# Performance work log

Measured on AMD Instinct MI355X. Metric: run time of the kernel, lower is better.

The kernel has to match this reference:

```python
import jax, jax.numpy as jnp
import numpy as np

NV, NSEG, SEGSZ, GRID = 778, 16, 49, 32
SCALE_FACTOR = 0.1


def grid_sample_3d(vol, pts):
    """Trilinear grid_sample, align_corners=True, zeros padding.
    vol: [D,H,W]; pts: [N,3] with (x,y,z) in [-1,1] (x indexes W, z indexes D).
    """
    D, H, W = vol.shape
    fx = (pts[:, 0] + 1.0) * 0.5 * (W - 1)
    fy = (pts[:, 1] + 1.0) * 0.5 * (H - 1)
    fz = (pts[:, 2] + 1.0) * 0.5 * (D - 1)
    x0f, y0f, z0f = jnp.floor(fx), jnp.floor(fy), jnp.floor(fz)
    wx, wy, wz = fx - x0f, fy - y0f, fz - z0f
    x0 = x0f.astype(jnp.int32)
    y0 = y0f.astype(jnp.int32)
    z0 = z0f.astype(jnp.int32)
    out = jnp.zeros(pts.shape[0], vol.dtype)
    for dz in (0, 1):
        zz = z0 + dz
        ww_z = wz if dz else (1.0 - wz)
        for dy in (0, 1):
            yy = y0 + dy
            ww_zy = ww_z * (wy if dy else (1.0 - wy))
            for dx in (0, 1):
                xx = x0 + dx
                w = ww_zy * (wx if dx else (1.0 - wx))
                valid = (xx >= 0) & (xx < W) & (yy >= 0) & (yy < H) & (zz >= 0) & (zz < D)
                v = vol[jnp.clip(zz, 0, D - 1), jnp.clip(yy, 0, H - 1), jnp.clip(xx, 0, W - 1)]
                out = out + jnp.where(valid, v, 0.0) * w
    return out


def _boxes(segv):
    # segv: [B,16,S,3] -> center [B,16,3], scale [B,16]  (no_grad in original)
    mn = segv.min(axis=2)
    mx = segv.max(axis=2)
    center = 0.5 * (mn + mx)                       # mean of (min, max)
    scale = (1.0 + SCALE_FACTOR) * 0.5 * (mx - mn).max(axis=-1)
    return jax.lax.stop_gradient(center), jax.lax.stop_gradient(scale)


def _cross_sample(seg_src, center, scale, phi, seg):
    # seg_src [B,I,S,3]; center [B,J,3]; scale [B,J]; phi [J,B,G,G,G]
    B = seg_src.shape[0]
    coords = (seg_src[:, :, None, :, :] - center[:, None, :, None, :]) / scale[:, None, :, None, None]
    pts = coords.transpose(2, 0, 1, 3, 4).reshape(NSEG, B, NSEG * SEGSZ, 3)  # [J,B,M,3]
    vals = jax.vmap(jax.vmap(grid_sample_3d))(phi, pts)                      # [J,B,M]
    vals = vals.reshape(NSEG, B, NSEG, SEGSZ).transpose(1, 2, 0, 3)          # [B,I,J,S]
    phisum = vals.sum(axis=2)                                                # [B,I,S]
    orisum = (vals * scale[:, None, :, None]).sum(axis=2)                    # [B,I,S]
    flat = seg.reshape(-1)
    out = jnp.zeros((B, NV), jnp.float32).at[:, flat].add(phisum.reshape(B, -1))
    ori = jnp.zeros((B, NV), jnp.float32).at[:, flat].add(orisum.reshape(B, -1))
    return out, ori


def setup_inputs() -> dict:
    key = jax.random.key(0)
    k1, k2, k3, k4 = jax.random.split(key, 4)
    bs = 128
    vertices = jax.random.normal(k1, (bs, 2, NV, 3), dtype=jnp.float32)
    seg = jax.random.randint(k2, (NSEG, SEGSZ), 0, NV).astype(jnp.int32)
    phi_right = jax.random.uniform(k3, (NSEG, bs, GRID, GRID, GRID), dtype=jnp.float32)
    phi_left = jax.random.uniform(k4, (NSEG, bs, GRID, GRID, GRID), dtype=jnp.float32)
    return {"vertices": vertices, "phi_right": phi_right, "phi_left": phi_left, "seg": seg}


def reference(vertices, phi_right, phi_left, seg):
    left_vert = vertices[:, 1]   # [B,778,3]
    right_vert = vertices[:, 0]
    segL = left_vert[:, seg]     # [B,16,S,3]
    segR = right_vert[:, seg]
    cL, sL = _boxes(segL)
    cR, sR = _boxes(segR)
    out_left, _ = _cross_sample(segL, cR, sR, phi_right, seg)
    out_right, _ = _cross_sample(segR, cL, sL, phi_left, seg)
    num_hand = 2
    loss = (out_left / num_hand ** 2 + out_right / num_hand ** 2).sum(axis=1)  # [B]
    return loss
```

## Files before the change

### kernel.cpp

```cpp
#include <hip/hip_runtime.h>

#define NVV   778
#define NSEG  16
#define SEGSZ 49
#define GRIDN 32
#define BATCH 128
#define NPTS  (NSEG * SEGSZ)
#define VOLSZ (GRIDN * GRIDN * GRIDN)

__global__ __launch_bounds__(1024) void sample_kernel(
    const float* __restrict__ vertices, const int* __restrict__ seg,
    const float* __restrict__ phiR, const float* __restrict__ phiL,
    float* __restrict__ loss)
{
    __shared__ float vol[VOLSZ];
    __shared__ float wsum[16];
    __shared__ float sbox[4];

    int blk  = blockIdx.x;
    int k    = blk % NSEG;
    int b    = (blk / NSEG) % BATCH;
    int pass = blk / (NSEG * BATCH);
    int srcSide = (pass == 0) ? 1 : 0;
    int boxSide = 1 - srcSide;
    const float* phi = (pass == 0 ? phiR : phiL) +
                       ((size_t)k * BATCH + b) * VOLSZ;
    const float* vsrc = vertices + ((size_t)b * 2 + srcSide) * NVV * 3;
    const float* vbox = vertices + ((size_t)b * 2 + boxSide) * NVV * 3;

    const int tid = threadIdx.x;

    float4 stg[8];
    #pragma unroll
    for (int i = 0; i < 8; ++i)
        stg[i] = *(const float4*)(phi + ((i * 1024 + tid) << 2));

    if (tid < 64) {
        bool act = tid < SEGSZ;
        int vi = act ? seg[k * SEGSZ + tid] : 0;
        const float* v = vbox + (size_t)vi * 3;
        float x = v[0], y = v[1], z = v[2];
        float mnx = act ? x : 1e30f, mxx = act ? x : -1e30f;
        float mny = act ? y : 1e30f, mxy = act ? y : -1e30f;
        float mnz = act ? z : 1e30f, mxz = act ? z : -1e30f;
        #pragma unroll
        for (int m = 32; m; m >>= 1) {
            mnx = fminf(mnx, __shfl_xor(mnx, m));
            mxx = fmaxf(mxx, __shfl_xor(mxx, m));
            mny = fminf(mny, __shfl_xor(mny, m));
            mxy = fmaxf(mxy, __shfl_xor(mxy, m));
            mnz = fminf(mnz, __shfl_xor(mnz, m));
            mxz = fmaxf(mxz, __shfl_xor(mxz, m));
        }
        if (tid == 0) {
            sbox[0] = 0.5f * (mnx + mxx);
            sbox[1] = 0.5f * (mny + mxy);
            sbox[2] = 0.5f * (mnz + mxz);
            float ext = fmaxf(fmaxf(mxx - mnx, mxy - mny), mxz - mnz);
            sbox[3] = 1.0f / (0.55f * ext);
        }
    }

    float vx = 0.f, vy = 0.f, vz = 0.f;
    if (tid < NPTS) {
        int vi = seg[tid];
        const float* v = vsrc + (size_t)vi * 3;
        vx = v[0]; vy = v[1]; vz = v[2];
    }

    #pragma unroll
    for (int i = 0; i < 8; ++i)
        *(float4*)&vol[(i * 1024 + tid) << 2] = stg[i];

    __syncthreads();

    float acc = 0.0f;
    if (tid < NPTS) {
        float cx = sbox[0], cy = sbox[1], cz = sbox[2], invs = sbox[3];
        float fx = ((vx - cx) * invs + 1.0f) * 15.5f;
        float fy = ((vy - cy) * invs + 1.0f) * 15.5f;
        float fz = ((vz - cz) * invs + 1.0f) * 15.5f;
        if (!(fx <= -1.0f || fx >= 32.0f ||
              fy <= -1.0f || fy >= 32.0f ||
              fz <= -1.0f || fz >= 32.0f)) {
            float x0f = floorf(fx), y0f = floorf(fy), z0f = floorf(fz);
            float wx = fx - x0f, wy = fy - y0f, wz = fz - z0f;
            int x0 = (int)x0f, y0 = (int)y0f, z0 = (int)z0f;
            #pragma unroll
            for (int dz = 0; dz < 2; ++dz) {
                int zz = z0 + dz;
                if (zz < 0 || zz >= GRIDN) continue;
                float wwz = dz ? wz : 1.0f - wz;
                #pragma unroll
                for (int dy = 0; dy < 2; ++dy) {
                    int yy = y0 + dy;
                    if (yy < 0 || yy >= GRIDN) continue;
                    float wzy = wwz * (dy ? wy : 1.0f - wy);
                    const float* row = vol + zz * (GRIDN * GRIDN) + yy * GRIDN;
                    #pragma unroll
                    for (int dx = 0; dx < 2; ++dx) {
                        int xx = x0 + dx;
                        if (xx < 0 || xx >= GRIDN) continue;
                        acc += wzy * (dx ? wx : 1.0f - wx) * row[xx];
                    }
                }
            }
        }
    }

    #pragma unroll
    for (int off = 32; off; off >>= 1)
        acc += __shfl_down(acc, off);
    int wid  = tid >> 6;
    int lane = tid & 63;
    if (lane == 0) wsum[wid] = acc;
    __syncthreads();
    if (tid == 0) {
        float tot = 0.f;
        #pragma unroll
        for (int i = 0; i < 16; ++i) tot += wsum[i];
        atomicAdd(loss + b, tot * 0.25f);
    }
}

extern "C" void kernel_launch(void* const* d_in, const int* in_sizes, int n_in,
                              void* d_out, int out_size, void* d_ws, size_t ws_size,
                              hipStream_t stream) {
    const float* vertices = (const float*)d_in[0];
    const float* phiR     = (const float*)d_in[1];
    const float* phiL     = (const float*)d_in[2];
    const int*   seg      = (const int*)d_in[3];
    float* loss = (float*)d_out;

    hipMemsetAsync(d_out, 0, (size_t)out_size * sizeof(float), stream);

    sample_kernel<<<2 * BATCH * NSEG, 1024, 0, stream>>>(
        vertices, seg, phiR, phiL, loss);
}
```

Before: 111.2 us.

## Make sampling kernel persistent and prefetch next volume into registers

The kernel now launches one block per CU, 256 in total, instead of one block per volume. Each block loops over 16 volumes. While the current volume is sampled from LDS, the next volume's global loads are issued into registers, so HBM traffic overlaps with sampling and the block-launch and LDS-fill latency is no longer exposed each time. The cost is a fixed mapping of work to blocks, which can leave CUs unevenly loaded, and register pressure from holding the prefetch buffer through the sampling phase.

```diff
diff --git a/kernel.cpp b/kernel.cpp
--- a/kernel.cpp
+++ b/kernel.cpp
@@ -7,6 +7,9 @@
 #define BATCH 128
 #define NPTS  (NSEG * SEGSZ)
 #define VOLSZ (GRIDN * GRIDN * GRIDN)
+#define NVOL  (2 * BATCH * NSEG)
+#define NBLK  256
+#define VPB   (NVOL / NBLK)
 
 __global__ __launch_bounds__(1024) void sample_kernel(
     const float* __restrict__ vertices, const int* __restrict__ seg,
@@ -17,109 +20,125 @@
     __shared__ float wsum[16];
     __shared__ float sbox[4];
 
-    int blk  = blockIdx.x;
-    int k    = blk % NSEG;
-    int b    = (blk / NSEG) % BATCH;
-    int pass = blk / (NSEG * BATCH);
-    int srcSide = (pass == 0) ? 1 : 0;
-    int boxSide = 1 - srcSide;
-    const float* phi = (pass == 0 ? phiR : phiL) +
-                       ((size_t)k * BATCH + b) * VOLSZ;
-    const float* vsrc = vertices + ((size_t)b * 2 + srcSide) * NVV * 3;
-    const float* vbox = vertices + ((size_t)b * 2 + boxSide) * NVV * 3;
-
     const int tid = threadIdx.x;
 
     float4 stg[8];
-    #pragma unroll
-    for (int i = 0; i < 8; ++i)
-        stg[i] = *(const float4*)(phi + ((i * 1024 + tid) << 2));
-
-    if (tid < 64) {
-        bool act = tid < SEGSZ;
-        int vi = act ? seg[k * SEGSZ + tid] : 0;
-        const float* v = vbox + (size_t)vi * 3;
-        float x = v[0], y = v[1], z = v[2];
-        float mnx = act ? x : 1e30f, mxx = act ? x : -1e30f;
-        float mny = act ? y : 1e30f, mxy = act ? y : -1e30f;
-        float mnz = act ? z : 1e30f, mxz = act ? z : -1e30f;
+    {
+        int vid  = blockIdx.x;
+        int k    = vid % NSEG;
+        int b    = (vid / NSEG) % BATCH;
+        int pass = vid / (NSEG * BATCH);
+        const float* phi = (pass == 0 ? phiR : phiL) +
+                           ((size_t)k * BATCH + b) * VOLSZ;
         #pragma unroll
-        for (int m = 32; m; m >>= 1) {
-            mnx = fminf(mnx, __shfl_xor(mnx, m));
-            mxx = fmaxf(mxx, __shfl_xor(mxx, m));
-            mny = fminf(mny, __shfl_xor(mny, m));
-            mxy = fmaxf(mxy, __shfl_xor(mxy, m));
-            mnz = fminf(mnz, __shfl_xor(mnz, m));
-            mxz = fmaxf(mxz, __shfl_xor(mxz, m));
-        }
-        if (tid == 0) {
-            sbox[0] = 0.5f * (mnx + mxx);
-            sbox[1] = 0.5f * (mny + mxy);
-            sbox[2] = 0.5f * (mnz + mxz);
-            float ext = fmaxf(fmaxf(mxx - mnx, mxy - mny), mxz - mnz);
-            sbox[3] = 1.0f / (0.55f * ext);
-        }
+        for (int i = 0; i < 8; ++i)
+            stg[i] = *(const float4*)(phi + ((i * 1024 + tid) << 2));
     }
 
-    float vx = 0.f, vy = 0.f, vz = 0.f;
-    if (tid < NPTS) {
-        int vi = seg[tid];
-        const float* v = vsrc + (size_t)vi * 3;
-        vx = v[0]; vy = v[1]; vz = v[2];
-    }
+    for (int it = 0; it < VPB; ++it) {
+        int vid  = blockIdx.x + NBLK * it;
+        int k    = vid % NSEG;
+        int b    = (vid / NSEG) % BATCH;
+        int pass = vid / (NSEG * BATCH);
+        int srcSide = (pass == 0) ? 1 : 0;
+        int boxSide = 1 - srcSide;
+        const float* vsrc = vertices + ((size_t)b * 2 + srcSide) * NVV * 3;
+        const float* vbox = vertices + ((size_t)b * 2 + boxSide) * NVV * 3;
 
-    #pragma unroll
-    for (int i = 0; i < 8; ++i)
-        *(float4*)&vol[(i * 1024 + tid) << 2] = stg[i];
+        if (tid < 64) {
+            bool act = tid < SEGSZ;
+            int vi = act ? seg[k * SEGSZ + tid] : 0;
+            const float* v = vbox + (size_t)vi * 3;
+            float x = v[0], y = v[1], z = v[2];
+            float mnx = act ? x : 1e30f, mxx = act ? x : -1e30f;
+            float mny = act ? y : 1e30f, mxy = act ? y : -1e30f;
+            float mnz = act ? z : 1e30f, mxz = act ? z : -1e30f;
+            #pragma unroll
+            for (int m = 32; m; m >>= 1) {
+                mnx = fminf(mnx, __shfl_xor(mnx, m));
+                mxx = fmaxf(mxx, __shfl_xor(mxx, m));
+                mny = fminf(mny, __shfl_xor(mny, m));
+                mxy = fmaxf(mxy, __shfl_xor(mxy, m));
+                mnz = fminf(mnz, __shfl_xor(mnz, m));
+                mxz = fmaxf(mxz, __shfl_xor(mxz, m));
+            }
+            if (tid == 0) {
+                sbox[0] = 0.5f * (mnx + mxx);
+                sbox[1] = 0.5f * (mny + mxy);
+                sbox[2] = 0.5f * (mnz + mxz);
+                float ext = fmaxf(fmaxf(mxx - mnx, mxy - mny), mxz - mnz);
+                sbox[3] = 1.0f / (0.55f * ext);
+            }
+        }
 
-    __syncthreads();
+        #pragma unroll
+        for (int i = 0; i < 8; ++i)
+            *(float4*)&vol[(i * 1024 + tid) << 2] = stg[i];
 
-    float acc = 0.0f;
-    if (tid < NPTS) {
-        float cx = sbox[0], cy = sbox[1], cz = sbox[2], invs = sbox[3];
-        float fx = ((vx - cx) * invs + 1.0f) * 15.5f;
-        float fy = ((vy - cy) * invs + 1.0f) * 15.5f;
-        float fz = ((vz - cz) * invs + 1.0f) * 15.5f;
-        if (!(fx <= -1.0f || fx >= 32.0f ||
-              fy <= -1.0f || fy >= 32.0f ||
-              fz <= -1.0f || fz >= 32.0f)) {
-            float x0f = floorf(fx), y0f = floorf(fy), z0f = floorf(fz);
-            float wx = fx - x0f, wy = fy - y0f, wz = fz - z0f;
-            int x0 = (int)x0f, y0 = (int)y0f, z0 = (int)z0f;
+        __syncthreads();
+
+        if (it + 1 < VPB) {
+            int nvid  = blockIdx.x + NBLK * (it + 1);
+            int nk    = nvid % NSEG;
+            int nb    = (nvid / NSEG) % BATCH;
+            int npass = nvid / (NSEG * BATCH);
+            const float* phin = (npass == 0 ? phiR : phiL) +
+                                ((size_t)nk * BATCH + nb) * VOLSZ;
             #pragma unroll
-            for (int dz = 0; dz < 2; ++dz) {
-                int zz = z0 + dz;
-                if (zz < 0 || zz >= GRIDN) continue;
-                float wwz = dz ? wz : 1.0f - wz;
+            for (int i = 0; i < 8; ++i)
+                stg[i] = *(const float4*)(phin + ((i * 1024 + tid) << 2));
+        }
+
+        float acc = 0.0f;
+        if (tid < NPTS) {
+            int vi = seg[tid];
+            const float* v = vsrc + (size_t)vi * 3;
+            float vx = v[0], vy = v[1], vz = v[2];
+            float cx = sbox[0], cy = sbox[1], cz = sbox[2], invs = sbox[3];
+            float fx = ((vx - cx) * invs + 1.0f) * 15.5f;
+            float fy = ((vy - cy) * invs + 1.0f) * 15.5f;
+            float fz = ((vz - cz) * invs + 1.0f) * 15.5f;
+            if (!(fx <= -1.0f || fx >= 32.0f ||
+                  fy <= -1.0f || fy >= 32.0f ||
+                  fz <= -1.0f || fz >= 32.0f)) {
+                float x0f = floorf(fx), y0f = floorf(fy), z0f = floorf(fz);
+                float wx = fx - x0f, wy = fy - y0f, wz = fz - z0f;
+                int x0 = (int)x0f, y0 = (int)y0f, z0 = (int)z0f;
                 #pragma unroll
-                for (int dy = 0; dy < 2; ++dy) {
-                    int yy = y0 + dy;
-                    if (yy < 0 || yy >= GRIDN) continue;
-                    float wzy = wwz * (dy ? wy : 1.0f - wy);
-                    const float* row = vol + zz * (GRIDN * GRIDN) + yy * GRIDN;
+                for (int dz = 0; dz < 2; ++dz) {
+                    int zz = z0 + dz;
+                    if (zz < 0 || zz >= GRIDN) continue;
+                    float wwz = dz ? wz : 1.0f - wz;
                     #pragma unroll
-                    for (int dx = 0; dx < 2; ++dx) {
-                        int xx = x0 + dx;
-                        if (xx < 0 || xx >= GRIDN) continue;
-                        acc += wzy * (dx ? wx : 1.0f - wx) * row[xx];
+                    for (int dy = 0; dy < 2; ++dy) {
+                        int yy = y0 + dy;
+                        if (yy < 0 || yy >= GRIDN) continue;
+                        float wzy = wwz * (dy ? wy : 1.0f - wy);
+                        const float* row = vol + zz * (GRIDN * GRIDN) + yy * GRIDN;
+                        #pragma unroll
+                        for (int dx = 0; dx < 2; ++dx) {
+                            int xx = x0 + dx;
+                            if (xx < 0 || xx >= GRIDN) continue;
+                            acc += wzy * (dx ? wx : 1.0f - wx) * row[xx];
+                        }
                     }
                 }
             }
         }
-    }
 
-    #pragma unroll
-    for (int off = 32; off; off >>= 1)
-        acc += __shfl_down(acc, off);
-    int wid  = tid >> 6;
-    int lane = tid & 63;
-    if (lane == 0) wsum[wid] = acc;
-    __syncthreads();
-    if (tid == 0) {
-        float tot = 0.f;
         #pragma unroll
-        for (int i = 0; i < 16; ++i) tot += wsum[i];
-        atomicAdd(loss + b, tot * 0.25f);
+        for (int off = 32; off; off >>= 1)
+            acc += __shfl_down(acc, off);
+        int wid  = tid >> 6;
+        int lane = tid & 63;
+        if (lane == 0) wsum[wid] = acc;
+        __syncthreads();
+        if (tid == 0) {
+            float tot = 0.f;
+            #pragma unroll
+            for (int i = 0; i < 16; ++i) tot += wsum[i];
+            atomicAdd(loss + b, tot * 0.25f);
+        }
     }
 }
 
@@ -134,6 +153,5 @@
 
     hipMemsetAsync(d_out, 0, (size_t)out_size * sizeof(float), stream);
 
-    sample_kernel<<<2 * BATCH * NSEG, 1024, 0, stream>>>(
-        vertices, seg, phiR, phiL, loss);
+    sample_kernel<<<NBLK, 1024, 0, stream>>>(vertices, seg, phiR, phiL, loss);
 }
```

After: 271.0 us. 2.44x slower.

## Make sampling kernel persistent with double-buffered volume prefetch

Applied to the files above, without the earlier changes.

Replaces one block per volume (4096 blocks) with 256 persistent blocks that each process 16 volumes. Register staging buffers prefetch the next volume from global memory while the current one is sampled out of LDS, and all 16 bounding boxes are computed up front, one per wave. The aim is to hide global-load latency and block launch and teardown costs behind compute in this bandwidth-bound kernel. The cost is much higher register pressure from two sets of eight float4 staging registers, and less parallelism available to the scheduler.

```diff
diff --git a/kernel.cpp b/kernel.cpp
--- a/kernel.cpp
+++ b/kernel.cpp
@@ -7,37 +7,123 @@
 #define BATCH 128
 #define NPTS  (NSEG * SEGSZ)
 #define VOLSZ (GRIDN * GRIDN * GRIDN)
+#define NVOL  (2 * BATCH * NSEG)
+#define NBLK  256
+#define VPB   (NVOL / NBLK)
 
-__global__ __launch_bounds__(1024) void sample_kernel(
+#define STG_ISSUE(S, P) \
+    S##0 = *(const float4*)((P) + 0 * 4096 + (tid << 2)); \
+    S##1 = *(const float4*)((P) + 1 * 4096 + (tid << 2)); \
+    S##2 = *(const float4*)((P) + 2 * 4096 + (tid << 2)); \
+    S##3 = *(const float4*)((P) + 3 * 4096 + (tid << 2)); \
+    S##4 = *(const float4*)((P) + 4 * 4096 + (tid << 2)); \
+    S##5 = *(const float4*)((P) + 5 * 4096 + (tid << 2)); \
+    S##6 = *(const float4*)((P) + 6 * 4096 + (tid << 2)); \
+    S##7 = *(const float4*)((P) + 7 * 4096 + (tid << 2));
+
+#define STG_COMMIT(S) \
+    *(float4*)&vol[0 * 4096 + (tid << 2)] = S##0; \
+    *(float4*)&vol[1 * 4096 + (tid << 2)] = S##1; \
+    *(float4*)&vol[2 * 4096 + (tid << 2)] = S##2; \
+    *(float4*)&vol[3 * 4096 + (tid << 2)] = S##3; \
+    *(float4*)&vol[4 * 4096 + (tid << 2)] = S##4; \
+    *(float4*)&vol[5 * 4096 + (tid << 2)] = S##5; \
+    *(float4*)&vol[6 * 4096 + (tid << 2)] = S##6; \
+    *(float4*)&vol[7 * 4096 + (tid << 2)] = S##7;
+
+#define PV_LOAD(IT, nx, ny, nz) \
+    if ((IT) < VPB && tid < NPTS) { \
+        int vid_ = bx + NBLK * (IT); \
+        int b_   = (vid_ >> 4) & (BATCH - 1); \
+        int src_ = (vid_ >> 11) == 0 ? 1 : 0; \
+        const float* v_ = vertices + (((size_t)b_ * 2 + src_) * NVV + pvi) * 3; \
+        nx = v_[0]; ny = v_[1]; nz = v_[2]; \
+    }
+
+#define TAPS_REDUCE(IT) { \
+    float acc = 0.0f; \
+    if (tid < NPTS) { \
+        float4 bx4 = sbox[IT]; \
+        float fx = ((pvx - bx4.x) * bx4.w + 1.0f) * 15.5f; \
+        float fy = ((pvy - bx4.y) * bx4.w + 1.0f) * 15.5f; \
+        float fz = ((pvz - bx4.z) * bx4.w + 1.0f) * 15.5f; \
+        if (!(fx <= -1.0f || fx >= 32.0f || \
+              fy <= -1.0f || fy >= 32.0f || \
+              fz <= -1.0f || fz >= 32.0f)) { \
+            float x0f = floorf(fx), y0f = floorf(fy), z0f = floorf(fz); \
+            float wx = fx - x0f, wy = fy - y0f, wz = fz - z0f; \
+            int x0 = (int)x0f, y0 = (int)y0f, z0 = (int)z0f; \
+            _Pragma("unroll") \
+            for (int dz = 0; dz < 2; ++dz) { \
+                int zz = z0 + dz; \
+                if (zz < 0 || zz >= GRIDN) continue; \
+                float wwz = dz ? wz : 1.0f - wz; \
+                _Pragma("unroll") \
+                for (int dy = 0; dy < 2; ++dy) { \
+                    int yy = y0 + dy; \
+                    if (yy < 0 || yy >= GRIDN) continue; \
+                    float wzy = wwz * (dy ? wy : 1.0f - wy); \
+                    const float* row = vol + zz * (GRIDN * GRIDN) + yy * GRIDN; \
+                    _Pragma("unroll") \
+                    for (int dx = 0; dx < 2; ++dx) { \
+                        int xx = x0 + dx; \
+                        if (xx < 0 || xx >= GRIDN) continue; \
+                        acc += wzy * (dx ? wx : 1.0f - wx) * row[xx]; \
+                    } \
+                } \
+            } \
+        } \
+    } \
+    _Pragma("unroll") \
+    for (int off = 32; off; off >>= 1) acc += __shfl_down(acc, off); \
+    if (lane == 0) wsum[wv] = acc; \
+    __syncthreads();  \
+    if (tid == 0) { \
+        float tot = 0.f; \
+        _Pragma("unroll") \
+        for (int i = 0; i < 16; ++i) tot += wsum[i]; \
+        int vid_ = bx + NBLK * (IT); \
+        atomicAdd(loss + ((vid_ >> 4) & (BATCH - 1)), tot * 0.25f); \
+    } }
+
+__global__ __launch_bounds__(1024, 4) void sample_kernel(
     const float* __restrict__ vertices, const int* __restrict__ seg,
     const float* __restrict__ phiR, const float* __restrict__ phiL,
     float* __restrict__ loss)
 {
     __shared__ float vol[VOLSZ];
+    __shared__ float4 sbox[VPB];
     __shared__ float wsum[16];
-    __shared__ float sbox[4];
-
-    int blk  = blockIdx.x;
-    int k    = blk % NSEG;
-    int b    = (blk / NSEG) % BATCH;
-    int pass = blk / (NSEG * BATCH);
-    int srcSide = (pass == 0) ? 1 : 0;
-    int boxSide = 1 - srcSide;
-    const float* phi = (pass == 0 ? phiR : phiL) +
-                       ((size_t)k * BATCH + b) * VOLSZ;
-    const float* vsrc = vertices + ((size_t)b * 2 + srcSide) * NVV * 3;
-    const float* vbox = vertices + ((size_t)b * 2 + boxSide) * NVV * 3;
 
     const int tid = threadIdx.x;
+    const int bx  = blockIdx.x;
+    const int k   = bx & (NSEG - 1);
+    const int wv  = tid >> 6;
+    const int lane = tid & 63;
 
-    float4 stg[8];
-    #pragma unroll
-    for (int i = 0; i < 8; ++i)
-        stg[i] = *(const float4*)(phi + ((i * 1024 + tid) << 2));
+    float4 a0, a1, a2, a3, a4, a5, a6, a7;
+    float4 b0, b1, b2, b3, b4, b5, b6, b7;
 
-    if (tid < 64) {
-        bool act = tid < SEGSZ;
-        int vi = act ? seg[k * SEGSZ + tid] : 0;
+    auto phiPtr = [&](int it) {
+        int vid  = bx + NBLK * it;
+        int b    = (vid >> 4) & (BATCH - 1);
+        int pass = vid >> 11;
+        return (pass == 0 ? phiR : phiL) + ((size_t)k * BATCH + b) * VOLSZ;
+    };
+
+    STG_ISSUE(a, phiPtr(0))
+    STG_ISSUE(b, phiPtr(1))
+
+    int pvi = (tid < NPTS) ? seg[tid] : 0;
+
+    {
+        int vid  = bx + NBLK * wv;
+        int bb   = (vid >> 4) & (BATCH - 1);
+        int pass = vid >> 11;
+        int boxSide = (pass == 0) ? 0 : 1;
+        const float* vbox = vertices + ((size_t)bb * 2 + boxSide) * NVV * 3;
+        bool act = lane < SEGSZ;
+        int vi = act ? seg[k * SEGSZ + lane] : 0;
         const float* v = vbox + (size_t)vi * 3;
         float x = v[0], y = v[1], z = v[2];
         float mnx = act ? x : 1e30f, mxx = act ? x : -1e30f;
@@ -52,74 +138,33 @@
             mnz = fminf(mnz, __shfl_xor(mnz, m));
             mxz = fmaxf(mxz, __shfl_xor(mxz, m));
         }
-        if (tid == 0) {
-            sbox[0] = 0.5f * (mnx + mxx);
-            sbox[1] = 0.5f * (mny + mxy);
-            sbox[2] = 0.5f * (mnz + mxz);
+        if (lane == 0) {
             float ext = fmaxf(fmaxf(mxx - mnx, mxy - mny), mxz - mnz);
-            sbox[3] = 1.0f / (0.55f * ext);
+            sbox[wv] = make_float4(0.5f * (mnx + mxx), 0.5f * (mny + mxy),
+                                   0.5f * (mnz + mxz), 1.0f / (0.55f * ext));
         }
     }
 
-    float vx = 0.f, vy = 0.f, vz = 0.f;
-    if (tid < NPTS) {
-        int vi = seg[tid];
-        const float* v = vsrc + (size_t)vi * 3;
-        vx = v[0]; vy = v[1]; vz = v[2];
-    }
-
-    #pragma unroll
-    for (int i = 0; i < 8; ++i)
-        *(float4*)&vol[(i * 1024 + tid) << 2] = stg[i];
+    float pvx = 0.f, pvy = 0.f, pvz = 0.f;
+    float nvx = 0.f, nvy = 0.f, nvz = 0.f;
+    PV_LOAD(0, pvx, pvy, pvz)
 
     __syncthreads();
 
-    float acc = 0.0f;
-    if (tid < NPTS) {
-        float cx = sbox[0], cy = sbox[1], cz = sbox[2], invs = sbox[3];
-        float fx = ((vx - cx) * invs + 1.0f) * 15.5f;
-        float fy = ((vy - cy) * invs + 1.0f) * 15.5f;
-        float fz = ((vz - cz) * invs + 1.0f) * 15.5f;
-        if (!(fx <= -1.0f || fx >= 32.0f ||
-              fy <= -1.0f || fy >= 32.0f ||
-              fz <= -1.0f || fz >= 32.0f)) {
-            float x0f = floorf(fx), y0f = floorf(fy), z0f = floorf(fz);
-            float wx = fx - x0f, wy = fy - y0f, wz = fz - z0f;
-            int x0 = (int)x0f, y0 = (int)y0f, z0 = (int)z0f;
-            #pragma unroll
-            for (int dz = 0; dz < 2; ++dz) {
-                int zz = z0 + dz;
-                if (zz < 0 || zz >= GRIDN) continue;
-                float wwz = dz ? wz : 1.0f - wz;
-                #pragma unroll
-                for (int dy = 0; dy < 2; ++dy) {
-                    int yy = y0 + dy;
-                    if (yy < 0 || yy >= GRIDN) continue;
-                    float wzy = wwz * (dy ? wy : 1.0f - wy);
-                    const float* row = vol + zz * (GRIDN * GRIDN) + yy * GRIDN;
-                    #pragma unroll
-                    for (int dx = 0; dx < 2; ++dx) {
-                        int xx = x0 + dx;
-                        if (xx < 0 || xx >= GRIDN) continue;
-                        acc += wzy * (dx ? wx : 1.0f - wx) * row[xx];
-                    }
-                }
-            }
-        }
-    }
+    for (int it = 0; it < VPB; it += 2) {
+        STG_COMMIT(a)
+        __syncthreads();
+        if (it + 2 < VPB) { STG_ISSUE(a, phiPtr(it + 2)) }
+        PV_LOAD(it + 1, nvx, nvy, nvz)
+        TAPS_REDUCE(it)
+        pvx = nvx; pvy = nvy; pvz = nvz;
 
-    #pragma unroll
-    for (int off = 32; off; off >>= 1)
-        acc += __shfl_down(acc, off);
-    int wid  = tid >> 6;
-    int lane = tid & 63;
-    if (lane == 0) wsum[wid] = acc;
-    __syncthreads();
-    if (tid == 0) {
-        float tot = 0.f;
-        #pragma unroll
-        for (int i = 0; i < 16; ++i) tot += wsum[i];
-        atomicAdd(loss + b, tot * 0.25f);
+        STG_COMMIT(b)
+        __syncthreads();
+        if (it + 3 < VPB) { STG_ISSUE(b, phiPtr(it + 3)) }
+        PV_LOAD(it + 2, nvx, nvy, nvz)
+        TAPS_REDUCE(it + 1)
+        pvx = nvx; pvy = nvy; pvz = nvz;
     }
 }
 
@@ -134,6 +179,5 @@
 
     hipMemsetAsync(d_out, 0, (size_t)out_size * sizeof(float), stream);
 
-    sample_kernel<<<2 * BATCH * NSEG, 1024, 0, stream>>>(
-        vertices, seg, phiR, phiL, loss);
+    sample_kernel<<<NBLK, 1024, 0, stream>>>(vertices, seg, phiR, phiL, loss);
 }
```

Measured after the change: 123.5 us. +11.0%, slower.

## Make sampler persistent with double-buffered async global-to-LDS volume streaming

Applied to the files above, without the earlier changes.

Replaces the one-block-per-volume launch (4096 blocks) with 256 persistent blocks that each process 16 volumes. Each volume is split into two LDS regions loaded with global_load_lds, and the next volume's first half streams in while the second half is still being sampled, so loads overlap compute. Box parameters for all 16 volumes are precomputed up front, one wave per volume. The cost is more complex synchronisation, a 15-slab split with duplicated boundary data, and only 256 blocks, which may underfill the GPU.

```diff
diff --git a/kernel.cpp b/kernel.cpp
--- a/kernel.cpp
+++ b/kernel.cpp
@@ -7,37 +7,99 @@
 #define BATCH 128
 #define NPTS  (NSEG * SEGSZ)
 #define VOLSZ (GRIDN * GRIDN * GRIDN)
+#define NVOL  (2 * BATCH * NSEG)
+#define NBLK  256
+#define VPB   (NVOL / NBLK)
 
-__global__ __launch_bounds__(1024) void sample_kernel(
+#define H0_FLOATS (16 * 1024)
+#define H1_FLOATS (17 * 1024)
+#define H0_CHUNKS (H0_FLOATS / 256)
+#define H1_CHUNKS (H1_FLOATS / 256)
+
+typedef __attribute__((address_space(1))) const void* as1_t;
+typedef __attribute__((address_space(3))) void* as3_t;
+
+#define STREAM(DST, SRC, NCH) \
+    for (int c = wv; c < (NCH); c += 16) { \
+        __builtin_amdgcn_global_load_lds( \
+            (as1_t)((SRC) + c * 256 + lane * 4), \
+            (as3_t)((DST) + c * 256), 16, 0, 0); \
+    }
+
+#define PV_LOAD(IT, nx, ny, nz) \
+    if ((IT) < VPB && tid < NPTS) { \
+        int vid_ = bx + NBLK * (IT); \
+        int b_   = (vid_ >> 4) & (BATCH - 1); \
+        int src_ = (vid_ >> 11) == 0 ? 1 : 0; \
+        const float* v_ = vertices + (((size_t)b_ * 2 + src_) * NVV + pvi) * 3; \
+        nx = v_[0]; ny = v_[1]; nz = v_[2]; \
+    }
+
+__device__ __forceinline__ float taps_half(
+    const float* base, int zrel0, bool z0ok, bool z1ok,
+    int x0, int y0, float wx, float wy, float wz)
+{
+    float s = 0.f;
+    #pragma unroll
+    for (int dz = 0; dz < 2; ++dz) {
+        if (!(dz ? z1ok : z0ok)) continue;
+        float wwz = dz ? wz : 1.f - wz;
+        const float* slab = base + (zrel0 + dz) * (GRIDN * GRIDN);
+        #pragma unroll
+        for (int dy = 0; dy < 2; ++dy) {
+            int yy = y0 + dy;
+            if (yy < 0 || yy >= GRIDN) continue;
+            float wzy = wwz * (dy ? wy : 1.f - wy);
+            const float* row = slab + yy * GRIDN;
+            #pragma unroll
+            for (int dx = 0; dx < 2; ++dx) {
+                int xx = x0 + dx;
+                if (xx < 0 || xx >= GRIDN) continue;
+                s += wzy * (dx ? wx : 1.f - wx) * row[xx];
+            }
+        }
+    }
+    return s;
+}
+
+__global__ __launch_bounds__(1024, 4) void sample_kernel(
     const float* __restrict__ vertices, const int* __restrict__ seg,
     const float* __restrict__ phiR, const float* __restrict__ phiL,
     float* __restrict__ loss)
 {
-    __shared__ float vol[VOLSZ];
+    __shared__ __align__(16) float R0[H0_FLOATS];
+    __shared__ __align__(16) float R1[H1_FLOATS];
+    __shared__ float4 sbox[VPB];
     __shared__ float wsum[16];
-    __shared__ float sbox[4];
 
-    int blk  = blockIdx.x;
-    int k    = blk % NSEG;
-    int b    = (blk / NSEG) % BATCH;
-    int pass = blk / (NSEG * BATCH);
-    int srcSide = (pass == 0) ? 1 : 0;
-    int boxSide = 1 - srcSide;
-    const float* phi = (pass == 0 ? phiR : phiL) +
-                       ((size_t)k * BATCH + b) * VOLSZ;
-    const float* vsrc = vertices + ((size_t)b * 2 + srcSide) * NVV * 3;
-    const float* vbox = vertices + ((size_t)b * 2 + boxSide) * NVV * 3;
+    const int tid  = threadIdx.x;
+    const int bx   = blockIdx.x;
+    const int k    = bx & (NSEG - 1);
+    const int wv   = tid >> 6;
+    const int lane = tid & 63;
 
-    const int tid = threadIdx.x;
+    auto phiPtr = [&](int it) {
+        int vid  = bx + NBLK * it;
+        int b    = (vid >> 4) & (BATCH - 1);
+        int pass = vid >> 11;
+        return (pass == 0 ? phiR : phiL) + ((size_t)k * BATCH + b) * VOLSZ;
+    };
 
-    float4 stg[8];
-    #pragma unroll
-    for (int i = 0; i < 8; ++i)
-        stg[i] = *(const float4*)(phi + ((i * 1024 + tid) << 2));
+    {
+        const float* p0 = phiPtr(0);
+        STREAM(R0, p0, H0_CHUNKS)
+    }
 
-    if (tid < 64) {
-        bool act = tid < SEGSZ;
-        int vi = act ? seg[k * SEGSZ + tid] : 0;
+    int pvi = (tid < NPTS) ? seg[tid] : 0;
+
+    {
+        int vid  = bx + NBLK * wv;
+        int bb   = (vid >> 4) & (BATCH - 1);
+        int pass = vid >> 11;
+        int boxSide = (pass == 0) ? 0 : 1;
+        const float* vbox = vertices + ((size_t)bb * 2 + boxSide) * NVV * 3;
+        bool act = lane < SEGSZ;
+        int vi = act ? seg[k * SEGSZ + lane] : 0;
         const float* v = vbox + (size_t)vi * 3;
         float x = v[0], y = v[1], z = v[2];
         float mnx = act ? x : 1e30f, mxx = act ? x : -1e30f;
@@ -52,74 +114,64 @@
             mnz = fminf(mnz, __shfl_xor(mnz, m));
             mxz = fmaxf(mxz, __shfl_xor(mxz, m));
         }
-        if (tid == 0) {
-            sbox[0] = 0.5f * (mnx + mxx);
-            sbox[1] = 0.5f * (mny + mxy);
-            sbox[2] = 0.5f * (mnz + mxz);
+        if (lane == 0) {
             float ext = fmaxf(fmaxf(mxx - mnx, mxy - mny), mxz - mnz);
-            sbox[3] = 1.0f / (0.55f * ext);
+            sbox[wv] = make_float4(0.5f * (mnx + mxx), 0.5f * (mny + mxy),
+                                   0.5f * (mnz + mxz), 1.0f / (0.55f * ext));
         }
     }
 
-    float vx = 0.f, vy = 0.f, vz = 0.f;
-    if (tid < NPTS) {
-        int vi = seg[tid];
-        const float* v = vsrc + (size_t)vi * 3;
-        vx = v[0]; vy = v[1]; vz = v[2];
-    }
-
-    #pragma unroll
-    for (int i = 0; i < 8; ++i)
-        *(float4*)&vol[(i * 1024 + tid) << 2] = stg[i];
+    float pvx = 0.f, pvy = 0.f, pvz = 0.f;
+    float nvx = 0.f, nvy = 0.f, nvz = 0.f;
+    PV_LOAD(0, pvx, pvy, pvz)
 
     __syncthreads();
 
-    float acc = 0.0f;
-    if (tid < NPTS) {
-        float cx = sbox[0], cy = sbox[1], cz = sbox[2], invs = sbox[3];
-        float fx = ((vx - cx) * invs + 1.0f) * 15.5f;
-        float fy = ((vy - cy) * invs + 1.0f) * 15.5f;
-        float fz = ((vz - cz) * invs + 1.0f) * 15.5f;
-        if (!(fx <= -1.0f || fx >= 32.0f ||
-              fy <= -1.0f || fy >= 32.0f ||
-              fz <= -1.0f || fz >= 32.0f)) {
-            float x0f = floorf(fx), y0f = floorf(fy), z0f = floorf(fz);
-            float wx = fx - x0f, wy = fy - y0f, wz = fz - z0f;
-            int x0 = (int)x0f, y0 = (int)y0f, z0 = (int)z0f;
+    for (int v = 0; v < VPB; ++v) {
+        const float* pv_phi = phiPtr(v);
+
+        STREAM(R1, pv_phi + 15 * 1024, H1_CHUNKS)
+
+        float fx = 0.f, fy = 0.f, fz = -2.f;
+        if (tid < NPTS) {
+            float4 b4 = sbox[v];
+            fx = ((pvx - b4.x) * b4.w + 1.f) * 15.5f;
+            fy = ((pvy - b4.y) * b4.w + 1.f) * 15.5f;
+            fz = ((pvz - b4.z) * b4.w + 1.f) * 15.5f;
+        }
+        PV_LOAD(v + 1, nvx, nvy, nvz)
+
+        bool inxy = (fx > -1.f && fx < 32.f && fy > -1.f && fy < 32.f);
+        float x0f = floorf(fx), y0f = floorf(fy), z0f = floorf(fz);
+        float wx = fx - x0f, wy = fy - y0f, wz = fz - z0f;
+        int x0 = (int)x0f, y0 = (int)y0f, z0 = (int)z0f;
+
+        float acc = 0.f;
+        if (inxy && fz > -1.f && fz < 15.f)
+            acc += taps_half(R0, z0, z0 >= 0, true, x0, y0, wx, wy, wz);
+
+        __syncthreads();
+
+        if (v + 1 < VPB) {
+            const float* pn_phi = phiPtr(v + 1);
+            STREAM(R0, pn_phi, H0_CHUNKS)
+        }
+        if (inxy && fz >= 15.f && fz < 32.f)
+            acc += taps_half(R1, z0 - 15, true, z0 + 1 < GRIDN, x0, y0, wx, wy, wz);
+
+        #pragma unroll
+        for (int off = 32; off; off >>= 1)
+            acc += __shfl_down(acc, off);
+        if (lane == 0) wsum[wv] = acc;
+        __syncthreads();
+        if (tid == 0) {
+            float tot = 0.f;
             #pragma unroll
-            for (int dz = 0; dz < 2; ++dz) {
-                int zz = z0 + dz;
-                if (zz < 0 || zz >= GRIDN) continue;
-                float wwz = dz ? wz : 1.0f - wz;
-                #pragma unroll
-                for (int dy = 0; dy < 2; ++dy) {
-                    int yy = y0 + dy;
-                    if (yy < 0 || yy >= GRIDN) continue;
-                    float wzy = wwz * (dy ? wy : 1.0f - wy);
-                    const float* row = vol + zz * (GRIDN * GRIDN) + yy * GRIDN;
-                    #pragma unroll
-                    for (int dx = 0; dx < 2; ++dx) {
-                        int xx = x0 + dx;
-                        if (xx < 0 || xx >= GRIDN) continue;
-                        acc += wzy * (dx ? wx : 1.0f - wx) * row[xx];
-                    }
-                }
-            }
+            for (int i = 0; i < 16; ++i) tot += wsum[i];
+            int vid = bx + NBLK * v;
+            atomicAdd(loss + ((vid >> 4) & (BATCH - 1)), tot * 0.25f);
         }
-    }
-
-    #pragma unroll
-    for (int off = 32; off; off >>= 1)
-        acc += __shfl_down(acc, off);
-    int wid  = tid >> 6;
-    int lane = tid & 63;
-    if (lane == 0) wsum[wid] = acc;
-    __syncthreads();
-    if (tid == 0) {
-        float tot = 0.f;
-        #pragma unroll
-        for (int i = 0; i < 16; ++i) tot += wsum[i];
-        atomicAdd(loss + b, tot * 0.25f);
+        pvx = nvx; pvy = nvy; pvz = nvz;
     }
 }
 
@@ -134,6 +186,5 @@
 
     hipMemsetAsync(d_out, 0, (size_t)out_size * sizeof(float), stream);
 
-    sample_kernel<<<2 * BATCH * NSEG, 1024, 0, stream>>>(
-        vertices, seg, phiR, phiL, loss);
+    sample_kernel<<<NBLK, 1024, 0, stream>>>(vertices, seg, phiR, phiL, loss);
 }
```

New measurement: 106.4 us. 1.05x faster.
